# Optimization experiments

Hardware: AMD Instinct MI355X
Metric: run time of the kernel (lower is better)

The kernel has to match this reference:

```python
import jax, jax.numpy as jnp
import numpy as np

B = 8192          # batch size
OBS = 128         # observation dim
HID = 512         # input_size / hidden_size
HEADS = 4         # num_input_heads
VSZ = 256         # input_value_size
NU = 64           # num_units (rim_num)
K = 8             # top-k
NOPT = 16         # option_num


def setup_inputs() -> dict:
    key = jax.random.key(0)
    ks = jax.random.split(key, 8)
    return {
        "x": jax.random.normal(ks[0], (B, OBS), dtype=jnp.float32),
        "option": jax.random.randint(ks[1], (B,), 0, NOPT),
        "pre_fc_w": jax.random.normal(ks[2], (OBS, HID), dtype=jnp.float32) * (OBS ** -0.5),
        "pre_fc_b": jax.random.normal(ks[3], (HID,), dtype=jnp.float32) * 0.01,
        "value_w": jax.random.normal(ks[4], (HID, HEADS * VSZ), dtype=jnp.float32) * (HID ** -0.5),
        "value_b": jax.random.normal(ks[5], (HEADS * VSZ,), dtype=jnp.float32) * 0.01,
        "p_w": jax.random.normal(ks[6], (NOPT, NU), dtype=jnp.float32),
        "p_b": jax.random.normal(ks[7], (NU,), dtype=jnp.float32),
    }


def reference(x, option, pre_fc_w, pre_fc_b, value_w, value_b, p_w, p_b):
    b = x.shape[0]
    # pre_fc: [B, OBS] -> [B, HID]
    h = x @ pre_fc_w + pre_fc_b
    # concat null input slot -> [B, 2, HID]
    h2 = jnp.stack([h, jnp.zeros_like(h)], axis=1)
    # one-hot option + null slot -> [B, 2, NOPT]
    oh = jax.nn.one_hot(option, NOPT, dtype=jnp.float32)
    oh2 = jnp.stack([oh, jnp.zeros_like(oh)], axis=1)
    # value projection, split heads, mean over heads -> [B, 2, VSZ]
    v = (h2 @ value_w + value_b).reshape(b, 2, HEADS, VSZ)
    value_layer = jnp.mean(v, axis=2)
    # attention scores: einsum('bio,on->bni') -> [B, NU, 2]
    scores = jnp.einsum('bio,on->bni', oh2, p_w)
    # bias: p_b for real slot, zeros for null slot
    pb = jnp.stack([jnp.broadcast_to(p_b, (b, NU)), jnp.zeros((b, NU), jnp.float32)], axis=2)
    scores = scores + pb
    # top-k unit mask over not-null scores [B, NU]
    not_null = scores[:, :, 0]
    _, topk_idx = jax.lax.top_k(not_null, K)  # [B, K]
    mask = jnp.zeros((b, NU), jnp.float32).at[jnp.arange(b)[:, None], topk_idx].set(1.0)
    # softmax over the 2 slots (dropout is identity at eval)
    probs = jax.nn.softmax(scores, axis=-1)  # [B, NU, 2]
    # attention readout, masked, mean over units -> [B, VSZ]
    inputs = jnp.einsum('bns,bsv->bnv', probs, value_layer) * mask[:, :, None]
    return jnp.mean(inputs, axis=1)
```

## Files before the change

### kernel.cpp

```cpp
#include <hip/hip_runtime.h>
#include <hip/hip_bf16.h>

#define B_N   8192
#define OBS   128
#define HID   512
#define VSZ   256
#define NU    64
#define TOPK  8
#define NOPT  16
#define KEXT  160

typedef __bf16 bf16_t;
typedef __bf16 bf16x8 __attribute__((ext_vector_type(8)));
typedef float  f32x4  __attribute__((ext_vector_type(4)));

#define OFF_A    0u
#define OFF_DP   256u
#define OFF_WT   2048u
#define OFF_MT   526336u

__global__ void k_pre(const float* __restrict__ vw, float* __restrict__ weff) {
    int j = blockIdx.x, v = threadIdx.x;
    const float* r = vw + j * (4 * VSZ);
    weff[j * VSZ + v] = 0.25f * ((r[v] + r[v + VSZ]) + (r[v + 2 * VSZ] + r[v + 3 * VSZ]));
}

__global__ void k_mt(const float* __restrict__ pw, const float* __restrict__ pb,
                     const float* __restrict__ weff, const float* __restrict__ p_w,
                     const float* __restrict__ p_b, const float* __restrict__ vb,
                     bf16_t* __restrict__ mt, float* __restrict__ A,
                     float* __restrict__ Dp) {
    const int tid = threadIdx.x;
    if (blockIdx.x == 129) {
        if (tid < VSZ) {
            bf16_t* row = mt + tid * KEXT;
            #pragma unroll
            for (int k = 129; k < KEXT; ++k) row[k] = (bf16_t)0.f;
        }
        int wvi = tid >> 6;
        if (wvi >= 4 && wvi < 8) {
            int lane = tid & 63;
            #pragma unroll
            for (int oo = 0; oo < 4; ++oo) {
                int o = (wvi - 4) * 4 + oo;
                float cur = p_w[o * NU + lane] + p_b[lane];
                float sum = 0.f;
                #pragma unroll
                for (int t = 0; t < TOPK; ++t) {
                    float m = cur;
                    #pragma unroll
                    for (int off = 32; off >= 1; off >>= 1)
                        m = fmaxf(m, __shfl_xor(m, off));
                    sum += 1.f / (1.f + expf(-m));
                    unsigned long long bal = __ballot(cur == m);
                    int first = __ffsll(bal) - 1;
                    if (lane == first) cur = -1e30f;
                }
                if (lane == 0) A[o] = sum * (1.f / NU);
            }
        }
        if (tid >= 512 && tid < 768) {
            int v = tid & 255;
            Dp[v] = 0.03125f * ((vb[v] + vb[v + VSZ]) + (vb[v + 2 * VSZ] + vb[v + 3 * VSZ]));
        }
        return;
    }

    int k  = blockIdx.x;
    int v  = tid & 255;
    int jq = tid >> 8;
    __shared__ float red[1024];
    const float* wr = (k < OBS) ? (pw + k * HID) : pb;
    const float* wj = wr + jq * 128;
    const float* wf = weff + (jq * 128) * VSZ + v;
    float a0 = 0.f, a1 = 0.f, a2 = 0.f, a3 = 0.f;
    #pragma unroll 4
    for (int j = 0; j < 128; j += 4) {
        a0 += wj[j + 0] * wf[(j + 0) * VSZ];
        a1 += wj[j + 1] * wf[(j + 1) * VSZ];
        a2 += wj[j + 2] * wf[(j + 2) * VSZ];
        a3 += wj[j + 3] * wf[(j + 3) * VSZ];
    }
    red[tid] = (a0 + a1) + (a2 + a3);
    __syncthreads();
    if (jq == 0)
        mt[v * KEXT + k] = (bf16_t)(((red[v] + red[v + 256]) + (red[v + 512] + red[v + 768])));
}

__launch_bounds__(256)
__global__ void k_main(const float* __restrict__ x, const bf16_t* __restrict__ mt,
                       const int* __restrict__ opt, const float* __restrict__ A,
                       const float* __restrict__ Dp, float* __restrict__ out) {
    const int wave = threadIdx.x >> 6;
    const int lane = threadIdx.x & 63;
    const int mrow = lane & 15;
    const int quad = lane >> 4;
    const int r0   = blockIdx.x * 64 + wave * 16;
    const int c0   = blockIdx.y * 128;

    bf16x8 af[5];
    {
        const float* xr = x + (r0 + mrow) * OBS + quad * 8;
        f32x4 lo[4], hi[4];
        #pragma unroll
        for (int kt = 0; kt < 4; ++kt) {
            lo[kt] = *(const f32x4*)(xr + kt * 32);
            hi[kt] = *(const f32x4*)(xr + kt * 32 + 4);
        }
        #pragma unroll
        for (int kt = 0; kt < 4; ++kt) {
            bf16x8 a;
            a[0] = (bf16_t)lo[kt][0]; a[1] = (bf16_t)lo[kt][1];
            a[2] = (bf16_t)lo[kt][2]; a[3] = (bf16_t)lo[kt][3];
            a[4] = (bf16_t)hi[kt][0]; a[5] = (bf16_t)hi[kt][1];
            a[6] = (bf16_t)hi[kt][2]; a[7] = (bf16_t)hi[kt][3];
            af[kt] = a;
        }
        bf16x8 a;
        #pragma unroll
        for (int j = 0; j < 8; ++j) a[j] = (bf16_t)0.f;
        if (quad == 0) a[0] = (bf16_t)1.0f;
        af[4] = a;
    }

    float av[4];
    #pragma unroll
    for (int r = 0; r < 4; ++r)
        av[r] = A[opt[r0 + quad * 4 + r]];

    f32x4 acc[8];
    #pragma unroll
    for (int t = 0; t < 8; ++t) acc[t] = (f32x4){0.f, 0.f, 0.f, 0.f};

    const bf16_t* mb = mt + (c0 + mrow) * KEXT + quad * 8;
    #pragma unroll
    for (int kt = 0; kt < 5; ++kt) {
        #pragma unroll
        for (int t = 0; t < 8; ++t) {
            bf16x8 b = *(const bf16x8*)(mb + t * 16 * KEXT + kt * 32);
            acc[t] = __builtin_amdgcn_mfma_f32_16x16x32_bf16(af[kt], b, acc[t], 0, 0, 0);
        }
    }

    #pragma unroll
    for (int r = 0; r < 4; ++r) {
        int row = r0 + quad * 4 + r;
        float* orow = out + row * VSZ;
        #pragma unroll
        for (int t = 0; t < 8; ++t) {
            int col = c0 + t * 16 + mrow;
            orow[col] = av[r] * acc[t][r] + Dp[col];
        }
    }
}

extern "C" void kernel_launch(void* const* d_in, const int* in_sizes, int n_in,
                              void* d_out, int out_size, void* d_ws, size_t ws_size,
                              hipStream_t stream) {
    const float* x        = (const float*)d_in[0];
    const int*   option   = (const int*)  d_in[1];
    const float* pre_fc_w = (const float*)d_in[2];
    const float* pre_fc_b = (const float*)d_in[3];
    const float* value_w  = (const float*)d_in[4];
    const float* value_b  = (const float*)d_in[5];
    const float* p_w      = (const float*)d_in[6];
    const float* p_b      = (const float*)d_in[7];
    float* out = (float*)d_out;

    char* ws = (char*)d_ws;
    float*  A    = (float*) (ws + OFF_A);
    float*  Dp   = (float*) (ws + OFF_DP);
    float*  weff = (float*) (ws + OFF_WT);
    bf16_t* mt   = (bf16_t*)(ws + OFF_MT);

    k_pre <<<dim3(HID), dim3(VSZ), 0, stream>>>(value_w, weff);
    k_mt  <<<dim3(130), dim3(1024), 0, stream>>>(pre_fc_w, pre_fc_b, weff,
                                                 p_w, p_b, value_b, mt, A, Dp);
    k_main<<<dim3(B_N / 64, VSZ / 128), dim3(256), 0, stream>>>(x, mt, option, A, Dp, out);
}
```

Baseline: 90.14 us.

## Fuse head-averaging of value weights into the combined weight precompute kernel

Merges the head-mean kernel and the pre_fc x value weight product into one kernel of 33 blocks. Each block computes an 8-column slice of the head-averaged value weights into LDS, then forms the 128x8 slice of the combined matrix plus the bias row. This removes one launch and the global round trip of the intermediate weff buffer. In exchange it uses far fewer blocks, so each thread does a longer serial 512-length dot product with less parallelism across the GPU.

```diff
diff --git a/kernel.cpp b/kernel.cpp
--- a/kernel.cpp
+++ b/kernel.cpp
@@ -16,33 +16,23 @@
 
 #define OFF_A    0u
 #define OFF_DP   256u
-#define OFF_WT   2048u
-#define OFF_MT   526336u
+#define OFF_MT   2048u
 
-__global__ void k_pre(const float* __restrict__ vw, float* __restrict__ weff) {
-    int j = blockIdx.x, v = threadIdx.x;
-    const float* r = vw + j * (4 * VSZ);
-    weff[j * VSZ + v] = 0.25f * ((r[v] + r[v + VSZ]) + (r[v + 2 * VSZ] + r[v + 3 * VSZ]));
-}
+__launch_bounds__(1024)
+__global__ void k_wmt(const float* __restrict__ vw, const float* __restrict__ pw,
+                      const float* __restrict__ pb, const float* __restrict__ p_w,
+                      const float* __restrict__ p_b, const float* __restrict__ vb,
+                      bf16_t* __restrict__ mt, float* __restrict__ A,
+                      float* __restrict__ Dp) {
+    const int tid = threadIdx.x;
 
-__global__ void k_mt(const float* __restrict__ pw, const float* __restrict__ pb,
-                     const float* __restrict__ weff, const float* __restrict__ p_w,
-                     const float* __restrict__ p_b, const float* __restrict__ vb,
-                     bf16_t* __restrict__ mt, float* __restrict__ A,
-                     float* __restrict__ Dp) {
-    const int tid = threadIdx.x;
-    if (blockIdx.x == 129) {
-        if (tid < VSZ) {
-            bf16_t* row = mt + tid * KEXT;
-            #pragma unroll
-            for (int k = 129; k < KEXT; ++k) row[k] = (bf16_t)0.f;
-        }
+    if (blockIdx.x == 32) {
         int wvi = tid >> 6;
-        if (wvi >= 4 && wvi < 8) {
+        if (wvi < 4) {
             int lane = tid & 63;
             #pragma unroll
             for (int oo = 0; oo < 4; ++oo) {
-                int o = (wvi - 4) * 4 + oo;
+                int o = wvi * 4 + oo;
                 float cur = p_w[o * NU + lane] + p_b[lane];
                 float sum = 0.f;
                 #pragma unroll
@@ -59,32 +49,61 @@
                 if (lane == 0) A[o] = sum * (1.f / NU);
             }
         }
-        if (tid >= 512 && tid < 768) {
+        if (tid >= 256 && tid < 512) {
             int v = tid & 255;
             Dp[v] = 0.03125f * ((vb[v] + vb[v + VSZ]) + (vb[v + 2 * VSZ] + vb[v + 3 * VSZ]));
         }
         return;
     }
 
-    int k  = blockIdx.x;
-    int v  = tid & 255;
-    int jq = tid >> 8;
-    __shared__ float red[1024];
-    const float* wr = (k < OBS) ? (pw + k * HID) : pb;
-    const float* wj = wr + jq * 128;
-    const float* wf = weff + (jq * 128) * VSZ + v;
-    float a0 = 0.f, a1 = 0.f, a2 = 0.f, a3 = 0.f;
-    #pragma unroll 4
-    for (int j = 0; j < 128; j += 4) {
-        a0 += wj[j + 0] * wf[(j + 0) * VSZ];
-        a1 += wj[j + 1] * wf[(j + 1) * VSZ];
-        a2 += wj[j + 2] * wf[(j + 2) * VSZ];
-        a3 += wj[j + 3] * wf[(j + 3) * VSZ];
+    __shared__ float wl[HID][8];
+    __shared__ float cpart[16][8];
+
+    const int v0 = blockIdx.x * 8;
+
+    #pragma unroll
+    for (int r = 0; r < 4; ++r) {
+        int e  = tid + r * 1024;
+        int j  = e >> 3, vi = e & 7;
+        const float* p = vw + j * (4 * VSZ) + v0 + vi;
+        wl[j][vi] = 0.25f * ((p[0] + p[VSZ]) + (p[2 * VSZ] + p[3 * VSZ]));
     }
-    red[tid] = (a0 + a1) + (a2 + a3);
     __syncthreads();
-    if (jq == 0)
-        mt[v * KEXT + k] = (bf16_t)(((red[v] + red[v + 256]) + (red[v + 512] + red[v + 768])));
+
+    {
+        int k  = tid >> 3, vi = tid & 7;
+        const float* pr = pw + k * HID;
+        float a0 = 0.f, a1 = 0.f, a2 = 0.f, a3 = 0.f;
+        #pragma unroll 4
+        for (int j = 0; j < HID; j += 4) {
+            f32x4 p = *(const f32x4*)(pr + j);
+            a0 += p[0] * wl[j + 0][vi];
+            a1 += p[1] * wl[j + 1][vi];
+            a2 += p[2] * wl[j + 2][vi];
+            a3 += p[3] * wl[j + 3][vi];
+        }
+        mt[(v0 + vi) * KEXT + k] = (bf16_t)((a0 + a1) + (a2 + a3));
+    }
+
+    if (tid < 128) {
+        int jq = tid >> 3, cvi = tid & 7;
+        const float* pbq = pb + jq * 32;
+        float s = 0.f;
+        #pragma unroll 4
+        for (int j = 0; j < 32; ++j) s += pbq[j] * wl[jq * 32 + j][cvi];
+        cpart[jq][cvi] = s;
+    }
+    __syncthreads();
+    if (tid < 8) {
+        float s = 0.f;
+        #pragma unroll
+        for (int q = 0; q < 16; ++q) s += cpart[q][tid];
+        mt[(v0 + tid) * KEXT + 128] = (bf16_t)s;
+    }
+    if (tid < 256) {
+        int pvi = tid >> 5, kk = tid & 31;
+        if (kk < 31) mt[(v0 + pvi) * KEXT + 129 + kk] = (bf16_t)0.f;
+    }
 }
 
 __launch_bounds__(256)
@@ -170,11 +189,9 @@
     char* ws = (char*)d_ws;
     float*  A    = (float*) (ws + OFF_A);
     float*  Dp   = (float*) (ws + OFF_DP);
-    float*  weff = (float*) (ws + OFF_WT);
     bf16_t* mt   = (bf16_t*)(ws + OFF_MT);
 
-    k_pre <<<dim3(HID), dim3(VSZ), 0, stream>>>(value_w, weff);
-    k_mt  <<<dim3(130), dim3(1024), 0, stream>>>(pre_fc_w, pre_fc_b, weff,
-                                                 p_w, p_b, value_b, mt, A, Dp);
+    k_wmt <<<dim3(33), dim3(1024), 0, stream>>>(value_w, pre_fc_w, pre_fc_b,
+                                                p_w, p_b, value_b, mt, A, Dp);
     k_main<<<dim3(B_N / 64, VSZ / 128), dim3(256), 0, stream>>>(x, mt, option, A, Dp, out);
 }
```

After: 94.82 us. 5.2% more time.
